# Kernel optimization log

Measured on AMD Instinct MI355X. Metric: run time of the kernel, lower is better.

Reference implementation:

```python
import jax, jax.numpy as jnp
import numpy as np

B, V, T = 1024, 50000, 50  # batch, n_items, max tail length

def setup_inputs() -> dict:
    key = jax.random.key(0)
    k1, k2, k3, k4 = jax.random.split(key, 4)
    output = jax.random.normal(k1, (B, V), dtype=jnp.float32)
    target = jax.random.randint(k2, (B,), 0, V, dtype=jnp.int32)
    tails = jax.random.randint(k3, (B, T), 0, V, dtype=jnp.int32)
    tail_len = jax.random.randint(k4, (B,), 0, T, dtype=jnp.int32)  # some rows have 0 -> empty tail
    return {"output": output, "target": target, "tails": tails, "tail_len": tail_len}


def reference(output, target, tails, tail_len):
    # output: [B, V] float scores; target: [B] int; tails: [B, T] padded indices; tail_len: [B]
    target_scores = jnp.take_along_axis(output, target[:, None].astype(jnp.int32), axis=1)[:, 0]  # [B]
    exp_out = jnp.exp(output)
    total_exp = jnp.sum(exp_out, axis=1)  # [B]  (torch: sum(exp(output), 1))
    log_pl = target_scores - jnp.log(total_exp)  # [B]

    # --- ragged tail term, vectorized over rows ---
    s = jnp.take_along_axis(output, tails, axis=1)          # [B, T] tail scores
    mask = jnp.arange(T)[None, :] < tail_len[:, None]       # [B, T] valid positions
    es = jnp.where(mask, jnp.exp(s), 0.0)                   # exp of valid tail scores
    above = jnp.sum(jnp.where(mask, s, 0.0), axis=1)        # [B] sum of tail scores
    # remaining mass: total - exp(target) - sum(exp(tail scores))
    others = total_exp - jnp.exp(target_scores) - jnp.sum(es, axis=1)  # [B]

    # torch flips the valid tail then cumsums exp; with padding at the end,
    # flipping the full padded row puts (zero-contribution) pads first, so the
    # cumsum at valid positions matches the valid-only reversed cumsum.
    fe = es[:, ::-1]                                        # [B, T]
    fmask = mask[:, ::-1]
    c = jnp.cumsum(fe, axis=1)                              # [B, T]
    lg = jnp.log(c + others[:, None])
    below_sum = jnp.sum(jnp.where(fmask, lg, 0.0), axis=1)  # [B]
    tail_term = jnp.where(tail_len > 0, above - below_sum, 0.0)  # rows with empty tail skipped

    neg_like = -(log_pl + tail_term)                        # [B]
    return neg_like
```

## Files before the change

### kernel.cpp

```cpp
#include <hip/hip_runtime.h>

#define BB 1024
#define VV 50000
#define TT 50

__global__ __launch_bounds__(256) void listmle_tail_kernel(
    const float* __restrict__ output,
    const int*   __restrict__ target,
    const int*   __restrict__ tails,
    const int*   __restrict__ tail_len,
    float*       __restrict__ out)
{
    const int b   = blockIdx.x;
    const int tid = threadIdx.x;
    const float* __restrict__ row = output + (size_t)b * VV;

    const float4* __restrict__ row4 = (const float4*)row;
    const int n4 = VV / 4;
    float sum = 0.0f;
    for (int i = tid; i < n4; i += 256) {
        float4 v = row4[i];
        sum += __expf(v.x) + __expf(v.y) + __expf(v.z) + __expf(v.w);
    }

    #pragma unroll
    for (int off = 32; off > 0; off >>= 1)
        sum += __shfl_down(sum, off, 64);

    __shared__ float wave_sums[4];
    __shared__ float total_exp_s;
    __shared__ float es_s[TT];
    __shared__ float s_s[TT];

    const int lane = tid & 63;
    const int wave = tid >> 6;
    if (lane == 0) wave_sums[wave] = sum;

    const int L = tail_len[b];
    if (tid < TT) {
        if (tid < L) {
            int idx = tails[b * TT + tid];
            float sv = row[idx];
            s_s[tid]  = sv;
            es_s[tid] = __expf(sv);
        } else {
            s_s[tid]  = 0.0f;
            es_s[tid] = 0.0f;
        }
    }
    __syncthreads();

    if (tid == 0) {
        total_exp_s = wave_sums[0] + wave_sums[1] + wave_sums[2] + wave_sums[3];
    }
    __syncthreads();

    if (tid == 0) {
        const float total_exp = total_exp_s;
        const float ts = row[target[b]];
        const float log_pl = ts - __logf(total_exp);

        float above = 0.0f, sum_es = 0.0f;
        for (int j = 0; j < L; ++j) {
            above  += s_s[j];
            sum_es += es_s[j];
        }
        const float others = total_exp - __expf(ts) - sum_es;

        float run = 0.0f, below = 0.0f;
        for (int k = L - 1; k >= 0; --k) {
            run += es_s[k];
            below += __logf(run + others);
        }
        const float tail_term = (L > 0) ? (above - below) : 0.0f;
        out[b] = -(log_pl + tail_term);
    }
}

extern "C" void kernel_launch(void* const* d_in, const int* in_sizes, int n_in,
                              void* d_out, int out_size, void* d_ws, size_t ws_size,
                              hipStream_t stream) {
    const float* output   = (const float*)d_in[0];
    const int*   target   = (const int*)d_in[1];
    const int*   tails    = (const int*)d_in[2];
    const int*   tail_len = (const int*)d_in[3];
    float*       out      = (float*)d_out;

    listmle_tail_kernel<<<BB, 256, 0, stream>>>(output, target, tails, tail_len, out);
}
```

Before: 287.7 us.

## Split row exp-sum across four blocks and move tail math to a second kernel

The single kernel becomes two. The first launches four blocks per row, each loading its quarter of the row with 12 unrolled float4 loads per thread and summing exponentials into four independent accumulators, then writing a partial sum to workspace. The second, a 64-thread kernel, combines the partials and computes the tail term. This raises parallelism and memory-level parallelism on the bandwidth-bound 200MB read, at the cost of an extra launch and a workspace round trip.

```diff
diff --git a/kernel.cpp b/kernel.cpp
--- a/kernel.cpp
+++ b/kernel.cpp
@@ -3,77 +3,103 @@
 #define BB 1024
 #define VV 50000
 #define TT 50
+#define Q4 3125
 
-__global__ __launch_bounds__(256) void listmle_tail_kernel(
+__global__ __launch_bounds__(256) void expsum_partial_kernel(
     const float* __restrict__ output,
-    const int*   __restrict__ target,
-    const int*   __restrict__ tails,
-    const int*   __restrict__ tail_len,
-    float*       __restrict__ out)
+    float*       __restrict__ partials)
 {
-    const int b   = blockIdx.x;
+    const int blk = blockIdx.x;
+    const int row = blk >> 2;
+    const int q   = blk & 3;
     const int tid = threadIdx.x;
-    const float* __restrict__ row = output + (size_t)b * VV;
+    const float4* __restrict__ p =
+        (const float4*)(output + (size_t)row * VV) + q * Q4;
 
-    const float4* __restrict__ row4 = (const float4*)row;
-    const int n4 = VV / 4;
-    float sum = 0.0f;
-    for (int i = tid; i < n4; i += 256) {
-        float4 v = row4[i];
-        sum += __expf(v.x) + __expf(v.y) + __expf(v.z) + __expf(v.w);
+    float4 v[12];
+    #pragma unroll
+    for (int u = 0; u < 12; ++u) v[u] = p[tid + 256 * u];
+    const bool has_tail = tid < (Q4 - 12 * 256);
+    float4 vt = make_float4(0.f, 0.f, 0.f, 0.f);
+    if (has_tail) vt = p[tid + 256 * 12];
+
+    float s0 = 0.f, s1 = 0.f, s2 = 0.f, s3 = 0.f;
+    #pragma unroll
+    for (int u = 0; u < 12; ++u) {
+        s0 += __expf(v[u].x);
+        s1 += __expf(v[u].y);
+        s2 += __expf(v[u].z);
+        s3 += __expf(v[u].w);
     }
+    if (has_tail) {
+        s0 += __expf(vt.x);
+        s1 += __expf(vt.y);
+        s2 += __expf(vt.z);
+        s3 += __expf(vt.w);
+    }
+    float sum = (s0 + s1) + (s2 + s3);
 
     #pragma unroll
     for (int off = 32; off > 0; off >>= 1)
         sum += __shfl_down(sum, off, 64);
 
-    __shared__ float wave_sums[4];
-    __shared__ float total_exp_s;
-    __shared__ float es_s[TT];
-    __shared__ float s_s[TT];
-
+    __shared__ float wsum[4];
     const int lane = tid & 63;
     const int wave = tid >> 6;
-    if (lane == 0) wave_sums[wave] = sum;
+    if (lane == 0) wsum[wave] = sum;
+    __syncthreads();
+    if (tid == 0)
+        partials[blk] = (wsum[0] + wsum[1]) + (wsum[2] + wsum[3]);
+}
 
-    const int L = tail_len[b];
+__global__ __launch_bounds__(64) void tail_kernel(
+    const float* __restrict__ output,
+    const int*   __restrict__ target,
+    const int*   __restrict__ tails,
+    const int*   __restrict__ tail_len,
+    const float* __restrict__ partials,
+    float*       __restrict__ out)
+{
+    const int r   = blockIdx.x;
+    const int tid = threadIdx.x;
+    const float* __restrict__ row = output + (size_t)r * VV;
+
+    __shared__ float s_s[TT];
+    __shared__ float es_s[TT];
+
+    const int L = tail_len[r];
     if (tid < TT) {
+        float sv = 0.f, ev = 0.f;
         if (tid < L) {
-            int idx = tails[b * TT + tid];
-            float sv = row[idx];
-            s_s[tid]  = sv;
-            es_s[tid] = __expf(sv);
-        } else {
-            s_s[tid]  = 0.0f;
-            es_s[tid] = 0.0f;
+            sv = row[tails[r * TT + tid]];
+            ev = __expf(sv);
         }
+        s_s[tid]  = sv;
+        es_s[tid] = ev;
     }
     __syncthreads();
 
     if (tid == 0) {
-        total_exp_s = wave_sums[0] + wave_sums[1] + wave_sums[2] + wave_sums[3];
-    }
-    __syncthreads();
+        const float total =
+            (partials[4 * r] + partials[4 * r + 1]) +
+            (partials[4 * r + 2] + partials[4 * r + 3]);
+        const float ts = row[target[r]];
+        const float log_pl = ts - __logf(total);
 
-    if (tid == 0) {
-        const float total_exp = total_exp_s;
-        const float ts = row[target[b]];
-        const float log_pl = ts - __logf(total_exp);
-
-        float above = 0.0f, sum_es = 0.0f;
+        float above = 0.f, sum_es = 0.f;
         for (int j = 0; j < L; ++j) {
             above  += s_s[j];
             sum_es += es_s[j];
         }
-        const float others = total_exp - __expf(ts) - sum_es;
+        const float others = total - __expf(ts) - sum_es;
 
-        float run = 0.0f, below = 0.0f;
+        float run = 0.f, below = 0.f;
         for (int k = L - 1; k >= 0; --k) {
             run += es_s[k];
             below += __logf(run + others);
         }
-        const float tail_term = (L > 0) ? (above - below) : 0.0f;
-        out[b] = -(log_pl + tail_term);
+        const float tail_term = (L > 0) ? (above - below) : 0.f;
+        out[r] = -(log_pl + tail_term);
     }
 }
 
@@ -85,6 +111,8 @@
     const int*   tails    = (const int*)d_in[2];
     const int*   tail_len = (const int*)d_in[3];
     float*       out      = (float*)d_out;
+    float*       partials = (float*)d_ws;
 
-    listmle_tail_kernel<<<BB, 256, 0, stream>>>(output, target, tails, tail_len, out);
+    expsum_partial_kernel<<<BB * 4, 256, 0, stream>>>(output, partials);
+    tail_kernel<<<BB, 64, 0, stream>>>(output, target, tails, tail_len, partials, out);
 }
```

Result: no change. 286.8 us (-0.3%).
